# Kernel optimization log

Measured on AMD Instinct MI355X. Metric: run time of the kernel, lower is better.

Reference implementation:

```python
import jax, jax.numpy as jnp
import numpy as np

ALPHA = 0.5

def pairwise_sqdist(a, b):
    # a: [B,N,3], b: [B,M,3] -> [B,N,M] squared euclidean distances
    a2 = jnp.sum(a * a, axis=-1)[:, :, None]
    b2 = jnp.sum(b * b, axis=-1)[:, None, :]
    ab = jnp.einsum('bnd,bmd->bnm', a, b)
    return jnp.maximum(a2 + b2 - 2.0 * ab, 0.0)

def setup_inputs() -> dict:
    key = jax.random.key(0)
    k1, k2, k3, k4, k5 = jax.random.split(key, 5)
    B, N_UP, N_SEED, N_GT, N_RAD = 4, 8192, 2048, 8192, 1024
    return {
        'pc_up':   jax.random.normal(k1, (B, N_UP, 3), dtype=jnp.float32),
        'pc_seed': jax.random.normal(k2, (B, N_SEED, 3), dtype=jnp.float32),
        'pc_conf': jax.random.uniform(k3, (B, N_RAD, 1), dtype=jnp.float32),
        'pc2':     jax.random.normal(k4, (B, N_GT, 3), dtype=jnp.float32),
        'pc3':     jax.random.normal(k5, (B, N_RAD, 3), dtype=jnp.float32),
    }

def reference(pc_up, pc_seed, pc_conf, pc2, pc3):
    # --- confidence score target: exp(-min euclidean dist from radar to GT) ---
    d_rad_gt = pairwise_sqdist(pc3, pc2)                      # [B,N_rad,N_gt]
    min_dist = jnp.sqrt(jnp.min(d_rad_gt, axis=-1))           # [B,N_rad]
    gt_scores = jnp.exp(-min_dist)[..., None]                 # [B,N_rad,1]
    conf_loss = jnp.mean((pc_conf - gt_scores) ** 2)

    # --- Chamfer (squared distances, as standard ChamferDistance kernels) ---
    d_up_gt = pairwise_sqdist(pc_up, pc2)                     # [B,N_up,N_gt]
    dist1 = jnp.min(d_up_gt, axis=2)                          # up -> gt
    dist2 = jnp.min(d_up_gt, axis=1)                          # gt -> up
    chamfer_up = 0.5 * jnp.mean(dist1) + 2.0 * jnp.mean(dist2)

    # --- EMD surrogate: nearest-neighbor matching cost, sqrt(dist).mean() ---
    # (original uses an approximate auction-based emdFunction; nearest-neighbor
    # assignment is the standard differentiable reference surrogate)
    emd_loss = jnp.mean(jnp.sqrt(dist1))

    final_loss = ALPHA * chamfer_up + ALPHA * conf_loss + emd_loss
    return final_loss
```

## Files before the change

kernel.cpp:

```cpp
#include <hip/hip_runtime.h>
#include <math.h>


#define THREADS 256
#define NSPLIT 8

typedef __attribute__((ext_vector_type(8))) short s8v;
typedef __attribute__((ext_vector_type(16))) float f16v;

__device__ __forceinline__ unsigned short f2bf(float x) {
    unsigned u = __float_as_uint(x);
    u += 0x7FFFu + ((u >> 16) & 1u);
    return (unsigned short)(u >> 16);
}
__device__ __forceinline__ float bf2f(unsigned short h) {
    return __uint_as_float((unsigned)h << 16);
}

__global__ __launch_bounds__(THREADS, 2) void
mfma_pass_kernel(const float* __restrict__ pc_up, const float* __restrict__ pc2,
                 const float* __restrict__ pc3,
                 float* p1, float* p2, float* p3) {
    __shared__ unsigned short tiles[32][2][32][8];

    int bid = blockIdx.x;
    const float* Ap;
    const float* Bp;
    float* part;
    int NA, rowsTot;
    if (bid < 512) {
        Ap = pc_up; Bp = pc2; part = p1; NA = 8192; rowsTot = 32768;
    } else if (bid < 1024) {
        bid -= 512; Ap = pc2; Bp = pc_up; part = p2; NA = 8192; rowsTot = 32768;
    } else {
        bid -= 1024; Ap = pc3; Bp = pc2; part = p3; NA = 1024; rowsTot = 4096;
    }
    const int rb = bid >> 3, sp = bid & 7;
    const int NB = 8192;
    const int rowBase = rb * 512;
    const int batch = rowBase / NA;
    const int colBase = sp * 1024;

    const float* bsrc = Bp + ((size_t)batch * NB + colBase) * 3;
    for (int c = threadIdx.x; c < 1024; c += THREADS) {
        float x = bsrc[c * 3 + 0], y = bsrc[c * 3 + 1], z = bsrc[c * 3 + 2];
        float ux = -2.f * x, uy = -2.f * y, uz = -2.f * z;
        unsigned short uxh = f2bf(ux), uyh = f2bf(uy), uzh = f2bf(uz);
        unsigned short uxl = f2bf(ux - bf2f(uxh));
        unsigned short uyl = f2bf(uy - bf2f(uyh));
        unsigned short uzl = f2bf(uz - bf2f(uzh));
        float b2 = x * x + y * y + z * z;
        unsigned short b2h = f2bf(b2);
        unsigned short b2l = f2bf(b2 - bf2f(b2h));
        int ct = c >> 5, cc = c & 31;
        s8v h0 = {(short)uxh, (short)uyh, (short)uzh, (short)uxh,
                  (short)uyh, (short)uzh, (short)uxl, (short)uyl};
        s8v h1 = {(short)uzl, (short)b2h, (short)b2l, 0, 0, 0, 0, 0};
        *(s8v*)&tiles[ct][0][cc][0] = h0;
        *(s8v*)&tiles[ct][1][cc][0] = h1;
    }

    const int lane = threadIdx.x & 63;
    const int w = threadIdx.x >> 6;
    const int half = lane >> 5;
    const int rl = lane & 31;
    s8v afrag[4];
    float a2[4];
#pragma unroll
    for (int f = 0; f < 4; ++f) {
        int row = rowBase + (w * 4 + f) * 32 + rl;
        float x = Ap[row * 3 + 0], y = Ap[row * 3 + 1], z = Ap[row * 3 + 2];
        unsigned short xh = f2bf(x), yh = f2bf(y), zh = f2bf(z);
        unsigned short xl = f2bf(x - bf2f(xh));
        unsigned short yl = f2bf(y - bf2f(yh));
        unsigned short zl = f2bf(z - bf2f(zh));
        a2[f] = x * x + y * y + z * z;
        s8v fr0 = {(short)xh, (short)yh, (short)zh, (short)xl,
                   (short)yl, (short)zl, (short)xh, (short)yh};
        s8v fr1 = {(short)zh, (short)0x3F80, (short)0x3F80, 0, 0, 0, 0, 0};
        afrag[f] = half ? fr1 : fr0;
    }
    __syncthreads();

    f16v zero;
#pragma unroll
    for (int i = 0; i < 16; ++i) zero[i] = 0.0f;
    float m[4] = {INFINITY, INFINITY, INFINITY, INFINITY};

#pragma unroll 2
    for (int t = 0; t < 32; ++t) {
        s8v bfrag = *(const s8v*)&tiles[t][half][rl][0];
#pragma unroll
        for (int f = 0; f < 4; ++f) {
            f16v d = __builtin_amdgcn_mfma_f32_32x32x16_bf16(
                bfrag, afrag[f], zero, 0, 0, 0);
            float u0 = fminf(fminf(d[0], d[1]), d[2]);
            float u1 = fminf(fminf(d[3], d[4]), d[5]);
            float u2 = fminf(fminf(d[6], d[7]), d[8]);
            float u3 = fminf(fminf(d[9], d[10]), d[11]);
            float u4 = fminf(fminf(d[12], d[13]), d[14]);
            float v0 = fminf(fminf(u0, u1), u2);
            float v1 = fminf(fminf(u3, u4), d[15]);
            m[f] = fminf(fminf(m[f], v0), v1);
        }
    }

#pragma unroll
    for (int f = 0; f < 4; ++f) {
        float v = fminf(m[f], __shfl_xor(m[f], 32, 64));
        float d = fmaxf(a2[f] + v, 0.0f);
        if (half == 0)
            part[sp * rowsTot + rowBase + (w * 4 + f) * 32 + rl] = d;
    }
}

__global__ __launch_bounds__(THREADS) void
reduce_kernel(const float* __restrict__ p1, const float* __restrict__ p2,
              const float* __restrict__ p3, const float* __restrict__ conf,
              float* __restrict__ out) {
    const int gid = blockIdx.x * THREADS + threadIdx.x;

    const float w1 = 0.25f / 32768.0f;
    const float wq = 1.0f / 32768.0f;
    const float w2 = 1.0f / 32768.0f;
    const float w3 = 0.5f / 4096.0f;

    float v1 = INFINITY, v2 = INFINITY;
#pragma unroll
    for (int sp = 0; sp < NSPLIT; ++sp) {
        v1 = fminf(v1, p1[sp * 32768 + gid]);
        v2 = fminf(v2, p2[sp * 32768 + gid]);
    }
    float s = w1 * v1 + wq * sqrtf(v1) + w2 * v2;
    if (gid < 4096) {
        float v3 = INFINITY;
#pragma unroll
        for (int sp = 0; sp < NSPLIT; ++sp)
            v3 = fminf(v3, p3[sp * 4096 + gid]);
        float diff = conf[gid] - expf(-sqrtf(v3));
        s += w3 * diff * diff;
    }

    __shared__ float wsum[4];
    const int lane = threadIdx.x & 63;
    const int wave = threadIdx.x >> 6;
    for (int off = 32; off > 0; off >>= 1) s += __shfl_down(s, off, 64);
    if (lane == 0) wsum[wave] = s;
    __syncthreads();
    if (threadIdx.x == 0)
        atomicAdd(out, wsum[0] + wsum[1] + wsum[2] + wsum[3]);
}

extern "C" void kernel_launch(void* const* d_in, const int* in_sizes, int n_in,
                              void* d_out, int out_size, void* d_ws, size_t ws_size,
                              hipStream_t stream) {
    const float* pc_up   = (const float*)d_in[0];
    const float* pc_conf = (const float*)d_in[2];
    const float* pc2     = (const float*)d_in[3];
    const float* pc3     = (const float*)d_in[4];

    float* p1 = (float*)d_ws;
    float* p2 = p1 + NSPLIT * 32768;
    float* p3 = p2 + NSPLIT * 32768;

    mfma_pass_kernel<<<1088, THREADS, 0, stream>>>(pc_up, pc2, pc3, p1, p2, p3);
    reduce_kernel<<<128, THREADS, 0, stream>>>(p1, p2, p3, pc_conf,
                                               (float*)d_out);
}
```

Measured before the change: 83.38 us.

## Hand-schedule MFMA min-distance loop in inline asm with smaller row tiles

Replaces the compiler-generated MFMA loop with hand-written inline assembly. It double-buffers LDS reads of B tiles, issues two MFMAs per step over different column tiles, and folds results with v_min3 into 16 running minima. Each block now handles 128 rows (one fragment per wave) instead of 512, so the grid grows to 4352 blocks and launch bounds allow 4 blocks per SM. The aim is to hide MFMA and LDS latency and cut per-element min overhead, at the cost of fragile hard-coded registers, fixed s_nop hazards, and rebuilding the B tile in LDS four times as often.

```diff
diff --git a/kernel.cpp b/kernel.cpp
--- a/kernel.cpp
+++ b/kernel.cpp
@@ -4,9 +4,9 @@
 
 #define THREADS 256
 #define NSPLIT 8
+#define COLS 1024
 
 typedef __attribute__((ext_vector_type(8))) short s8v;
-typedef __attribute__((ext_vector_type(16))) float f16v;
 
 __device__ __forceinline__ unsigned short f2bf(float x) {
     unsigned u = __float_as_uint(x);
@@ -17,7 +17,32 @@
     return __uint_as_float((unsigned)h << 16);
 }
 
-__global__ __launch_bounds__(THREADS, 2) void
+#define RD_A "ds_read_b128 v[48:51], v84 offset:0\n" \
+             "ds_read_b128 v[52:55], v84 offset:1024\n" \
+             "v_add_u32 v84, 2048, v84\n"
+#define RD_B "ds_read_b128 v[56:59], v84 offset:0\n" \
+             "ds_read_b128 v[60:63], v84 offset:1024\n" \
+             "v_add_u32 v84, 2048, v84\n"
+#define FOLD16 \
+    "s_nop 7\n" "s_nop 7\n" \
+    "v_min3_f32 v0, v0, v16, v32\n"   "v_min3_f32 v1, v1, v17, v33\n" \
+    "v_min3_f32 v2, v2, v18, v34\n"   "v_min3_f32 v3, v3, v19, v35\n" \
+    "v_min3_f32 v4, v4, v20, v36\n"   "v_min3_f32 v5, v5, v21, v37\n" \
+    "v_min3_f32 v6, v6, v22, v38\n"   "v_min3_f32 v7, v7, v23, v39\n" \
+    "v_min3_f32 v8, v8, v24, v40\n"   "v_min3_f32 v9, v9, v25, v41\n" \
+    "v_min3_f32 v10, v10, v26, v42\n" "v_min3_f32 v11, v11, v27, v43\n" \
+    "v_min3_f32 v12, v12, v28, v44\n" "v_min3_f32 v13, v13, v29, v45\n" \
+    "v_min3_f32 v14, v14, v30, v46\n" "v_min3_f32 v15, v15, v31, v47\n"
+#define MF_A(W) "s_waitcnt lgkmcnt(" W ")\n" \
+    "v_mfma_f32_32x32x16_bf16 v[16:31], v[48:51], v[80:83], v[64:79]\n" \
+    "v_mfma_f32_32x32x16_bf16 v[32:47], v[52:55], v[80:83], v[64:79]\n"
+#define MF_B(W) "s_waitcnt lgkmcnt(" W ")\n" \
+    "v_mfma_f32_32x32x16_bf16 v[16:31], v[56:59], v[80:83], v[64:79]\n" \
+    "v_mfma_f32_32x32x16_bf16 v[32:47], v[60:63], v[80:83], v[64:79]\n"
+#define BODY_ODD  RD_A FOLD16 MF_B("2")
+#define BODY_EVEN RD_B FOLD16 MF_A("2")
+
+__global__ __launch_bounds__(THREADS, 4) void
 mfma_pass_kernel(const float* __restrict__ pc_up, const float* __restrict__ pc2,
                  const float* __restrict__ pc3,
                  float* p1, float* p2, float* p3) {
@@ -28,21 +53,21 @@
     const float* Bp;
     float* part;
     int NA, rowsTot;
-    if (bid < 512) {
+    if (bid < 2048) {
         Ap = pc_up; Bp = pc2; part = p1; NA = 8192; rowsTot = 32768;
-    } else if (bid < 1024) {
-        bid -= 512; Ap = pc2; Bp = pc_up; part = p2; NA = 8192; rowsTot = 32768;
+    } else if (bid < 4096) {
+        bid -= 2048; Ap = pc2; Bp = pc_up; part = p2; NA = 8192; rowsTot = 32768;
     } else {
-        bid -= 1024; Ap = pc3; Bp = pc2; part = p3; NA = 1024; rowsTot = 4096;
+        bid -= 4096; Ap = pc3; Bp = pc2; part = p3; NA = 1024; rowsTot = 4096;
     }
     const int rb = bid >> 3, sp = bid & 7;
     const int NB = 8192;
-    const int rowBase = rb * 512;
+    const int rowBase = rb * 128;
     const int batch = rowBase / NA;
-    const int colBase = sp * 1024;
+    const int colBase = sp * COLS;
 
     const float* bsrc = Bp + ((size_t)batch * NB + colBase) * 3;
-    for (int c = threadIdx.x; c < 1024; c += THREADS) {
+    for (int c = threadIdx.x; c < COLS; c += THREADS) {
         float x = bsrc[c * 3 + 0], y = bsrc[c * 3 + 1], z = bsrc[c * 3 + 2];
         float ux = -2.f * x, uy = -2.f * y, uz = -2.f * z;
         unsigned short uxh = f2bf(ux), uyh = f2bf(uy), uzh = f2bf(uz);
@@ -64,54 +89,76 @@
     const int w = threadIdx.x >> 6;
     const int half = lane >> 5;
     const int rl = lane & 31;
-    s8v afrag[4];
-    float a2[4];
-#pragma unroll
-    for (int f = 0; f < 4; ++f) {
-        int row = rowBase + (w * 4 + f) * 32 + rl;
-        float x = Ap[row * 3 + 0], y = Ap[row * 3 + 1], z = Ap[row * 3 + 2];
-        unsigned short xh = f2bf(x), yh = f2bf(y), zh = f2bf(z);
-        unsigned short xl = f2bf(x - bf2f(xh));
-        unsigned short yl = f2bf(y - bf2f(yh));
-        unsigned short zl = f2bf(z - bf2f(zh));
-        a2[f] = x * x + y * y + z * z;
-        s8v fr0 = {(short)xh, (short)yh, (short)zh, (short)xl,
-                   (short)yl, (short)zl, (short)xh, (short)yh};
-        s8v fr1 = {(short)zh, (short)0x3F80, (short)0x3F80, 0, 0, 0, 0, 0};
-        afrag[f] = half ? fr1 : fr0;
-    }
+    const int row = rowBase + w * 32 + rl;
+    float x = Ap[row * 3 + 0], y = Ap[row * 3 + 1], z = Ap[row * 3 + 2];
+    unsigned xh = f2bf(x), yh = f2bf(y), zh = f2bf(z);
+    unsigned xl = f2bf(x - bf2f((unsigned short)xh));
+    unsigned yl = f2bf(y - bf2f((unsigned short)yh));
+    unsigned zl = f2bf(z - bf2f((unsigned short)zh));
+    float a2 = x * x + y * y + z * z;
+    unsigned f0d0 = xh | (yh << 16), f0d1 = zh | (xl << 16);
+    unsigned f0d2 = yl | (zl << 16), f0d3 = xh | (yh << 16);
+    unsigned f1d0 = zh | (0x3F80u << 16), f1d1 = 0x3F80u;
+    unsigned af0 = half ? f1d0 : f0d0;
+    unsigned af1 = half ? f1d1 : f0d1;
+    unsigned af2 = half ? 0u : f0d2;
+    unsigned af3 = half ? 0u : f0d3;
+    unsigned lds_addr = (unsigned)(size_t)&tiles[0][half][rl][0];
     __syncthreads();
 
-    f16v zero;
-#pragma unroll
-    for (int i = 0; i < 16; ++i) zero[i] = 0.0f;
-    float m[4] = {INFINITY, INFINITY, INFINITY, INFINITY};
-
-#pragma unroll 2
-    for (int t = 0; t < 32; ++t) {
-        s8v bfrag = *(const s8v*)&tiles[t][half][rl][0];
-#pragma unroll
-        for (int f = 0; f < 4; ++f) {
-            f16v d = __builtin_amdgcn_mfma_f32_32x32x16_bf16(
-                bfrag, afrag[f], zero, 0, 0, 0);
-            float u0 = fminf(fminf(d[0], d[1]), d[2]);
-            float u1 = fminf(fminf(d[3], d[4]), d[5]);
-            float u2 = fminf(fminf(d[6], d[7]), d[8]);
-            float u3 = fminf(fminf(d[9], d[10]), d[11]);
-            float u4 = fminf(fminf(d[12], d[13]), d[14]);
-            float v0 = fminf(fminf(u0, u1), u2);
-            float v1 = fminf(fminf(u3, u4), d[15]);
-            m[f] = fminf(fminf(m[f], v0), v1);
-        }
-    }
-
-#pragma unroll
-    for (int f = 0; f < 4; ++f) {
-        float v = fminf(m[f], __shfl_xor(m[f], 32, 64));
-        float d = fmaxf(a2[f] + v, 0.0f);
-        if (half == 0)
-            part[sp * rowsTot + rowBase + (w * 4 + f) * 32 + rl] = d;
-    }
+    float m;
+    asm volatile(
+        "v_mov_b32 v80, %1\n" "v_mov_b32 v81, %2\n"
+        "v_mov_b32 v82, %3\n" "v_mov_b32 v83, %4\n"
+        "v_mov_b32 v84, %5\n"
+        "v_mov_b32 v0, 0x7f800000\n"  "v_mov_b32 v1, 0x7f800000\n"
+        "v_mov_b32 v2, 0x7f800000\n"  "v_mov_b32 v3, 0x7f800000\n"
+        "v_mov_b32 v4, 0x7f800000\n"  "v_mov_b32 v5, 0x7f800000\n"
+        "v_mov_b32 v6, 0x7f800000\n"  "v_mov_b32 v7, 0x7f800000\n"
+        "v_mov_b32 v8, 0x7f800000\n"  "v_mov_b32 v9, 0x7f800000\n"
+        "v_mov_b32 v10, 0x7f800000\n" "v_mov_b32 v11, 0x7f800000\n"
+        "v_mov_b32 v12, 0x7f800000\n" "v_mov_b32 v13, 0x7f800000\n"
+        "v_mov_b32 v14, 0x7f800000\n" "v_mov_b32 v15, 0x7f800000\n"
+        "v_mov_b32 v64, 0\n" "v_mov_b32 v65, 0\n" "v_mov_b32 v66, 0\n"
+        "v_mov_b32 v67, 0\n" "v_mov_b32 v68, 0\n" "v_mov_b32 v69, 0\n"
+        "v_mov_b32 v70, 0\n" "v_mov_b32 v71, 0\n" "v_mov_b32 v72, 0\n"
+        "v_mov_b32 v73, 0\n" "v_mov_b32 v74, 0\n" "v_mov_b32 v75, 0\n"
+        "v_mov_b32 v76, 0\n" "v_mov_b32 v77, 0\n" "v_mov_b32 v78, 0\n"
+        "v_mov_b32 v79, 0\n"
+        RD_A
+        RD_B MF_A("2")
+        BODY_ODD BODY_EVEN
+        BODY_ODD BODY_EVEN
+        BODY_ODD BODY_EVEN
+        BODY_ODD BODY_EVEN
+        BODY_ODD BODY_EVEN
+        BODY_ODD BODY_EVEN
+        BODY_ODD BODY_EVEN
+        FOLD16 MF_B("0")
+        FOLD16
+        "v_min3_f32 v16, v0, v1, v2\n"
+        "v_min3_f32 v17, v3, v4, v5\n"
+        "v_min3_f32 v18, v6, v7, v8\n"
+        "v_min3_f32 v19, v9, v10, v11\n"
+        "v_min3_f32 v20, v12, v13, v14\n"
+        "v_min3_f32 v21, v16, v17, v18\n"
+        "v_min3_f32 v22, v19, v20, v15\n"
+        "v_min_f32 %0, v21, v22\n"
+        : "=&v"(m)
+        : "v"(af0), "v"(af1), "v"(af2), "v"(af3), "v"(lds_addr)
+        : "v0","v1","v2","v3","v4","v5","v6","v7","v8","v9","v10","v11",
+          "v12","v13","v14","v15","v16","v17","v18","v19","v20","v21","v22",
+          "v23","v24","v25","v26","v27","v28","v29","v30","v31","v32","v33",
+          "v34","v35","v36","v37","v38","v39","v40","v41","v42","v43","v44",
+          "v45","v46","v47","v48","v49","v50","v51","v52","v53","v54","v55",
+          "v56","v57","v58","v59","v60","v61","v62","v63","v64","v65","v66",
+          "v67","v68","v69","v70","v71","v72","v73","v74","v75","v76","v77",
+          "v78","v79","v80","v81","v82","v83","v84","memory");
+
+    float v = fminf(m, __shfl_xor(m, 32, 64));
+    float d = fmaxf(a2 + v, 0.0f);
+    if (half == 0)
+        part[sp * rowsTot + row] = d;
 }
 
 __global__ __launch_bounds__(THREADS) void
@@ -163,7 +210,7 @@
     float* p2 = p1 + NSPLIT * 32768;
     float* p3 = p2 + NSPLIT * 32768;
 
-    mfma_pass_kernel<<<1088, THREADS, 0, stream>>>(pc_up, pc2, pc3, p1, p2, p3);
+    mfma_pass_kernel<<<4352, THREADS, 0, stream>>>(pc_up, pc2, pc3, p1, p2, p3);
     reduce_kernel<<<128, THREADS, 0, stream>>>(p1, p2, p3, pc_conf,
                                                (float*)d_out);
 }
```

Result: slower. 90.04 us (+8.0%).
